# Performance work log

Hardware: AMD Instinct MI355X
Metric: run time of the kernel (lower is better)

## Reference

```python
import jax, jax.numpy as jnp
import numpy as np

B, L_IN, D = 4, 4096, 1024
R_MIN, R_MAX = 0.9, 0.999


def setup_inputs() -> dict:
    key = jax.random.key(0)
    k0, k1, k2 = jax.random.split(key, 3)
    inputs = jax.random.normal(k0, (B, L_IN, D), jnp.float32)
    Wi = jax.random.normal(k1, (2 * D, D), jnp.float32) / np.sqrt(D)
    bi = jnp.zeros((2 * D,), jnp.float32)
    Wo = jax.random.normal(k2, (D, 2 * D), jnp.float32) / np.sqrt(2 * D)
    bo = jnp.zeros((D,), jnp.float32)
    # LRU stable-ring initialization, exactly as in the torch module
    rng = np.random.default_rng(0)
    u1 = rng.random(D)
    u2 = rng.random(D)
    v_log = np.log(-0.5 * np.log(u1 * (R_MAX ** 2 - R_MIN ** 2) + R_MIN ** 2))
    theta_log = np.log(u2 * np.pi * 2)
    gamma_log = np.log(np.sqrt(1.0 - np.exp(-np.exp(v_log)) ** 2))
    params_log = jnp.asarray(np.stack([v_log, theta_log, gamma_log]), jnp.float32)
    return {"inputs": inputs, "Wi": Wi, "bi": bi, "Wo": Wo, "bo": bo,
            "params_log": params_log}


def _lru_forward(inputs, Wi, bi, Wo, bo, params_log):
    b, l_in, d = inputs.shape
    u = inputs @ Wi.T + bi                      # [B, L, 2D]
    v, theta, gamma = jnp.exp(params_log)       # each [D]
    # torch.view_as_complex: interleaved (real, imag) pairs along last dim
    uc = u.reshape(b, l_in, d, 2)
    x = jax.lax.complex(uc[..., 0], uc[..., 1])  # [B, L, D] complex64
    log2_L = int(np.ceil(np.log2(l_in)))
    L = 2 ** log2_L
    x = jnp.pad(x, ((0, 0), (0, L - l_in), (0, 0)))
    # Blelloch-style log-depth scan: x_t = lambda * x_{t-1} + u_t,
    # lambda = exp(-v + i*theta)
    for i in range(1, log2_L + 1):
        blk = 2 ** i
        xb = x.reshape(b * L // blk, blk, d)
        x1, x2 = xb[:, : blk // 2], xb[:, blk // 2:]
        pos = jnp.arange(1, blk // 2 + 1, dtype=jnp.float32)  # [blk/2]
        lambs = jnp.exp(jax.lax.complex(-pos[:, None] * v,
                                        pos[:, None] * theta))  # [blk/2, D]
        x2 = x2 + lambs * x1[:, -1:]
        x = jnp.concatenate([x1, x2], axis=1).reshape(b, L, d)
    x = x[:, :l_in] * gamma.astype(x.dtype)     # normalize, drop padding
    xr = jnp.concatenate([x.real, x.imag], axis=-1)  # [B, L, 2D]
    out = xr @ Wo.T + bo
    return jax.nn.relu(out)


def reference(inputs, Wi, bi, Wo, bo, params_log):
    return _lru_forward(inputs, Wi, bi, Wo, bo, params_log)
```

## Files before the change

### kernel.cpp

```cpp
#include <hip/hip_runtime.h>

#define BB 4
#define LL 4096
#define DD 1024
#define SS2 128
#define TT2 32

typedef __attribute__((ext_vector_type(4))) float  floatx4;
typedef __attribute__((ext_vector_type(8))) short  shortx8;

static __device__ __forceinline__ unsigned short f2bf(float f) {
    unsigned int u = __float_as_uint(f);
    u += 0x7fffu + ((u >> 16) & 1u);
    return (unsigned short)(u >> 16);
}
static __device__ __forceinline__ float bf2f(unsigned short h) {
    return __uint_as_float(((unsigned int)h) << 16);
}

#define NIN4 (BB * LL * DD / 4)
#define NW4  (2 * DD * DD / 4)
__global__ void cast_all_kernel(const float4* __restrict__ s_in, ushort4* __restrict__ d_inb,
                                const float4* __restrict__ s_wi, ushort4* __restrict__ d_wib,
                                const float4* __restrict__ s_wo, ushort4* __restrict__ d_wob) {
    int i = blockIdx.x * blockDim.x + threadIdx.x;
    const float4* s; ushort4* d; int j;
    if (i < NIN4)                 { s = s_in; d = d_inb; j = i; }
    else if (i < NIN4 + NW4)      { s = s_wi; d = d_wib; j = i - NIN4; }
    else                          { s = s_wo; d = d_wob; j = i - NIN4 - NW4; }
    float4 v = s[j];
    ushort4 o;
    o.x = f2bf(v.x); o.y = f2bf(v.y); o.z = f2bf(v.z); o.w = f2bf(v.w);
    d[j] = o;
}

template<int K, int NT, int EPI>
__global__ __launch_bounds__(256)
void gemm_bt(const unsigned short* __restrict__ A,
             const unsigned short* __restrict__ B,
             const float* __restrict__ bias,
             void* __restrict__ Cp) {
    constexpr int N = NT * 128;
    __shared__ __align__(16) short As[128 * 64];
    __shared__ __align__(16) short Bs[128 * 64];

    const int tid = threadIdx.x;
    const int b   = blockIdx.x;
    const int xcd = b & 7;
    const int i2  = b >> 3;
    const int tileM = ((i2 / NT) * 8 + xcd) * 128;
    const int tileN = (i2 % NT) * 128;

    const int lane  = tid & 63;
    const int wave  = tid >> 6;
    const int wm    = (wave >> 1) * 64;
    const int wn    = (wave & 1) * 64;
    const int r16   = lane & 15;
    const int quad  = lane >> 4;

    floatx4 acc[4][4] = {};

    int rowS[4], colS[4];
#pragma unroll
    for (int n = 0; n < 4; ++n) {
        const int q = tid + n * 256;
        rowS[n] = q >> 3;
        colS[n] = ((q & 7) ^ (rowS[n] & 7)) * 8;
    }
    const int ldsBase = (tid & ~63) * 8;

    const int fx = r16 & 7;

    for (int k0 = 0; k0 < K; k0 += 64) {
#pragma unroll
        for (int n = 0; n < 4; ++n) {
            __builtin_amdgcn_global_load_lds(
                (const __attribute__((address_space(1))) void*)&A[(size_t)(tileM + rowS[n]) * K + k0 + colS[n]],
                (__attribute__((address_space(3))) void*)&As[ldsBase + n * 2048], 16, 0, 0);
            __builtin_amdgcn_global_load_lds(
                (const __attribute__((address_space(1))) void*)&B[(size_t)(tileN + rowS[n]) * K + k0 + colS[n]],
                (__attribute__((address_space(3))) void*)&Bs[ldsBase + n * 2048], 16, 0, 0);
        }
        __syncthreads();

#pragma unroll
        for (int kk = 0; kk < 2; ++kk) {
            const int slot = ((kk * 4 + quad) ^ fx) * 8;
            shortx8 af[4], bfv[4];
#pragma unroll
            for (int i = 0; i < 4; ++i)
                af[i] = *(const shortx8*)(&As[(wm + i * 16 + r16) * 64 + slot]);
#pragma unroll
            for (int j = 0; j < 4; ++j)
                bfv[j] = *(const shortx8*)(&Bs[(wn + j * 16 + r16) * 64 + slot]);
#pragma unroll
            for (int i = 0; i < 4; ++i)
#pragma unroll
                for (int j = 0; j < 4; ++j)
                    acc[i][j] = __builtin_amdgcn_mfma_f32_16x16x32_bf16(
                        af[i], bfv[j], acc[i][j], 0, 0, 0);
        }
        __syncthreads();
    }

#pragma unroll
    for (int i = 0; i < 4; ++i) {
#pragma unroll
        for (int j = 0; j < 4; ++j) {
            const int col = tileN + wn + j * 16 + r16;
            const float bv = bias[col];
#pragma unroll
            for (int r = 0; r < 4; ++r) {
                const int row = tileM + wm + i * 16 + quad * 4 + r;
                float v = acc[i][j][r] + bv;
                if (EPI == 0) {
                    ((unsigned short*)Cp)[(size_t)row * N + col] = f2bf(v);
                } else {
                    ((float*)Cp)[(size_t)row * N + col] = fmaxf(v, 0.0f);
                }
            }
        }
    }
}

__global__ __launch_bounds__(256)
void scanA(const unsigned short* __restrict__ u,
           const float* __restrict__ plog,
           float2* __restrict__ Eend) {
    const int d0 = (blockIdx.x * 256 + threadIdx.x) * 2;
    const int c = blockIdx.y, b = blockIdx.z;
    const float v0  = expf(plog[d0]),      v1  = expf(plog[d0 + 1]);
    const float th0 = expf(plog[DD + d0]), th1 = expf(plog[DD + d0 + 1]);
    const float a0 = expf(-v0), a1 = expf(-v1);
    const float lr0 = a0 * cosf(th0), li0 = a0 * sinf(th0);
    const float lr1 = a1 * cosf(th1), li1 = a1 * sinf(th1);

    uint2 uc[TT2];
    const unsigned short* up = u + (size_t)(b * LL + c * TT2) * (2 * DD) + 2 * d0;
#pragma unroll
    for (int t = 0; t < TT2; ++t)
        uc[t] = *(const uint2*)(up + (size_t)t * (2 * DD));

    float zr0 = 0.f, zi0 = 0.f, zr1 = 0.f, zi1 = 0.f;
#pragma unroll
    for (int t = 0; t < TT2; ++t) {
        float xr0 = bf2f((unsigned short)(uc[t].x & 0xffffu));
        float xi0 = bf2f((unsigned short)(uc[t].x >> 16));
        float xr1 = bf2f((unsigned short)(uc[t].y & 0xffffu));
        float xi1 = bf2f((unsigned short)(uc[t].y >> 16));
        float w;
        w = lr0 * zr0 - li0 * zi0 + xr0; zi0 = lr0 * zi0 + li0 * zr0 + xi0; zr0 = w;
        w = lr1 * zr1 - li1 * zi1 + xr1; zi1 = lr1 * zi1 + li1 * zr1 + xi1; zr1 = w;
    }
    *(float4*)&Eend[(size_t)c * (BB * DD) + b * DD + d0] =
        make_float4(zr0, zi0, zr1, zi1);
}

__global__ __launch_bounds__(256)
void scanC(const unsigned short* __restrict__ u,
           const float* __restrict__ plog,
           const float2* __restrict__ Eend,
           unsigned short* __restrict__ xr) {
    const int d0 = (blockIdx.x * 256 + threadIdx.x) * 2;
    const int c = blockIdx.y, b = blockIdx.z;
    const float v0  = expf(plog[d0]),      v1  = expf(plog[d0 + 1]);
    const float th0 = expf(plog[DD + d0]), th1 = expf(plog[DD + d0 + 1]);
    const float g0  = expf(plog[2 * DD + d0]), g1 = expf(plog[2 * DD + d0 + 1]);
    const float a0 = expf(-v0), a1 = expf(-v1);
    const float lr0 = a0 * cosf(th0), li0 = a0 * sinf(th0);
    const float lr1 = a1 * cosf(th1), li1 = a1 * sinf(th1);

    uint2 uc[TT2];
    const unsigned short* up = u + (size_t)(b * LL + c * TT2) * (2 * DD) + 2 * d0;
#pragma unroll
    for (int t = 0; t < TT2; ++t)
        uc[t] = *(const uint2*)(up + (size_t)t * (2 * DD));

    const float aT0 = expf(-(float)TT2 * v0), aT1 = expf(-(float)TT2 * v1);
    const float Lr0 = aT0 * cosf((float)TT2 * th0), Li0 = aT0 * sinf((float)TT2 * th0);
    const float Lr1 = aT1 * cosf((float)TT2 * th1), Li1 = aT1 * sinf((float)TT2 * th1);
    float yr0 = 0.f, yi0 = 0.f, yr1 = 0.f, yi1 = 0.f;
    for (int cc = 0; cc < c; ++cc) {
        float4 e = *(const float4*)&Eend[(size_t)cc * (BB * DD) + b * DD + d0];
        float w;
        w = Lr0 * yr0 - Li0 * yi0 + e.x; yi0 = Lr0 * yi0 + Li0 * yr0 + e.y; yr0 = w;
        w = Lr1 * yr1 - Li1 * yi1 + e.z; yi1 = Lr1 * yi1 + Li1 * yr1 + e.w; yr1 = w;
    }

    unsigned short* xp = xr + (size_t)(b * LL + c * TT2) * (2 * DD) + d0;
#pragma unroll
    for (int t = 0; t < TT2; ++t) {
        float xr0 = bf2f((unsigned short)(uc[t].x & 0xffffu));
        float xi0 = bf2f((unsigned short)(uc[t].x >> 16));
        float xr1 = bf2f((unsigned short)(uc[t].y & 0xffffu));
        float xi1 = bf2f((unsigned short)(uc[t].y >> 16));
        float w;
        w = lr0 * yr0 - li0 * yi0 + xr0; yi0 = lr0 * yi0 + li0 * yr0 + xi0; yr0 = w;
        w = lr1 * yr1 - li1 * yi1 + xr1; yi1 = lr1 * yi1 + li1 * yr1 + xi1; yr1 = w;
        *(unsigned int*)&xp[(size_t)t * (2 * DD)] =
            (unsigned int)f2bf(g0 * yr0) | ((unsigned int)f2bf(g1 * yr1) << 16);
        *(unsigned int*)&xp[(size_t)t * (2 * DD) + DD] =
            (unsigned int)f2bf(g0 * yi0) | ((unsigned int)f2bf(g1 * yi1) << 16);
    }
}

extern "C" void kernel_launch(void* const* d_in, const int* in_sizes, int n_in,
                              void* d_out, int out_size, void* d_ws, size_t ws_size,
                              hipStream_t stream) {
    const float* inputs = (const float*)d_in[0];
    const float* Wi     = (const float*)d_in[1];
    const float* bi     = (const float*)d_in[2];
    const float* Wo     = (const float*)d_in[3];
    const float* bo     = (const float*)d_in[4];
    const float* plog   = (const float*)d_in[5];
    float* out = (float*)d_out;

    const size_t M = (size_t)BB * LL;
    unsigned short* u_bf  = (unsigned short*)d_ws;
    unsigned short* xr_bf = u_bf  + M * 2 * DD;
    unsigned short* in_bf = xr_bf + M * 2 * DD;
    unsigned short* Wi_bf = in_bf + M * DD;
    unsigned short* Wo_bf = Wi_bf + (size_t)2 * DD * DD;
    float2* Eend = (float2*)(Wo_bf + (size_t)2 * DD * DD);

    {
        int total4 = NIN4 + 2 * NW4;
        cast_all_kernel<<<total4 / 256, 256, 0, stream>>>(
            (const float4*)inputs, (ushort4*)in_bf,
            (const float4*)Wi,     (ushort4*)Wi_bf,
            (const float4*)Wo,     (ushort4*)Wo_bf);
    }

    gemm_bt<DD, 16, 0><<<(M / 128) * 16, 256, 0, stream>>>(
        in_bf, Wi_bf, bi, (void*)u_bf);

    scanA<<<dim3(DD / 512, SS2, BB), 256, 0, stream>>>(u_bf, plog, Eend);
    scanC<<<dim3(DD / 512, SS2, BB), 256, 0, stream>>>(u_bf, plog, Eend, xr_bf);

    gemm_bt<2 * DD, 8, 1><<<(M / 128) * 8, 256, 0, stream>>>(
        xr_bf, Wo_bf, bo, (void*)out);
}
```

Measured before the change: 359.7 us.

## Add a chunk-carry scan kernel so scanC reads precomputed carries

Adds a scanB kernel that sequentially scans the per-chunk end states across the 128 chunks once per (batch, channel pair) and writes each chunk's incoming carry. scanC then loads its carry directly instead of re-running a loop over all preceding chunks, which previously gave quadratic total work and uneven load across blocks. The cost is an extra kernel launch, a small serial kernel with only 8 blocks, and extra workspace for the carries.

After: 339.2 us. -5.7%, faster.

```diff
diff --git a/kernel.cpp b/kernel.cpp
--- a/kernel.cpp
+++ b/kernel.cpp
@@ -157,9 +157,43 @@
 }
 
 __global__ __launch_bounds__(256)
+void scanB(const float2* __restrict__ Eend,
+           const float* __restrict__ plog,
+           float2* __restrict__ Cin) {
+    const int idx = blockIdx.x * 256 + threadIdx.x;
+    const int b  = idx / (DD / 2);
+    const int d0 = (idx % (DD / 2)) * 2;
+    const float v0  = expf(plog[d0]),      v1  = expf(plog[d0 + 1]);
+    const float th0 = expf(plog[DD + d0]), th1 = expf(plog[DD + d0 + 1]);
+    const float aT0 = expf(-(float)TT2 * v0), aT1 = expf(-(float)TT2 * v1);
+    const float Lr0 = aT0 * cosf((float)TT2 * th0), Li0 = aT0 * sinf((float)TT2 * th0);
+    const float Lr1 = aT1 * cosf((float)TT2 * th1), Li1 = aT1 * sinf((float)TT2 * th1);
+
+    const size_t base = (size_t)b * DD + d0;
+    float yr0 = 0.f, yi0 = 0.f, yr1 = 0.f, yi1 = 0.f;
+#pragma unroll
+    for (int g = 0; g < SS2 / 16; ++g) {
+        float4 eb[16], cb[16];
+#pragma unroll
+        for (int t = 0; t < 16; ++t)
+            eb[t] = *(const float4*)&Eend[(size_t)(g * 16 + t) * (BB * DD) + base];
+#pragma unroll
+        for (int t = 0; t < 16; ++t) {
+            cb[t] = make_float4(yr0, yi0, yr1, yi1);
+            float w;
+            w = Lr0 * yr0 - Li0 * yi0 + eb[t].x; yi0 = Lr0 * yi0 + Li0 * yr0 + eb[t].y; yr0 = w;
+            w = Lr1 * yr1 - Li1 * yi1 + eb[t].z; yi1 = Lr1 * yi1 + Li1 * yr1 + eb[t].w; yr1 = w;
+        }
+#pragma unroll
+        for (int t = 0; t < 16; ++t)
+            *(float4*)&Cin[(size_t)(g * 16 + t) * (BB * DD) + base] = cb[t];
+    }
+}
+
+__global__ __launch_bounds__(256)
 void scanC(const unsigned short* __restrict__ u,
            const float* __restrict__ plog,
-           const float2* __restrict__ Eend,
+           const float2* __restrict__ Cin,
            unsigned short* __restrict__ xr) {
     const int d0 = (blockIdx.x * 256 + threadIdx.x) * 2;
     const int c = blockIdx.y, b = blockIdx.z;
@@ -176,16 +210,8 @@
     for (int t = 0; t < TT2; ++t)
         uc[t] = *(const uint2*)(up + (size_t)t * (2 * DD));
 
-    const float aT0 = expf(-(float)TT2 * v0), aT1 = expf(-(float)TT2 * v1);
-    const float Lr0 = aT0 * cosf((float)TT2 * th0), Li0 = aT0 * sinf((float)TT2 * th0);
-    const float Lr1 = aT1 * cosf((float)TT2 * th1), Li1 = aT1 * sinf((float)TT2 * th1);
-    float yr0 = 0.f, yi0 = 0.f, yr1 = 0.f, yi1 = 0.f;
-    for (int cc = 0; cc < c; ++cc) {
-        float4 e = *(const float4*)&Eend[(size_t)cc * (BB * DD) + b * DD + d0];
-        float w;
-        w = Lr0 * yr0 - Li0 * yi0 + e.x; yi0 = Lr0 * yi0 + Li0 * yr0 + e.y; yr0 = w;
-        w = Lr1 * yr1 - Li1 * yi1 + e.z; yi1 = Lr1 * yi1 + Li1 * yr1 + e.w; yr1 = w;
-    }
+    float4 cy = *(const float4*)&Cin[(size_t)c * (BB * DD) + b * DD + d0];
+    float yr0 = cy.x, yi0 = cy.y, yr1 = cy.z, yi1 = cy.w;
 
     unsigned short* xp = xr + (size_t)(b * LL + c * TT2) * (2 * DD) + d0;
 #pragma unroll
@@ -222,6 +248,7 @@
     unsigned short* Wi_bf = in_bf + M * DD;
     unsigned short* Wo_bf = Wi_bf + (size_t)2 * DD * DD;
     float2* Eend = (float2*)(Wo_bf + (size_t)2 * DD * DD);
+    float2* Cin  = Eend + (size_t)SS2 * BB * DD;
 
     {
         int total4 = NIN4 + 2 * NW4;
@@ -235,7 +262,8 @@
         in_bf, Wi_bf, bi, (void*)u_bf);
 
     scanA<<<dim3(DD / 512, SS2, BB), 256, 0, stream>>>(u_bf, plog, Eend);
-    scanC<<<dim3(DD / 512, SS2, BB), 256, 0, stream>>>(u_bf, plog, Eend, xr_bf);
+    scanB<<<(BB * DD / 2) / 256, 256, 0, stream>>>(Eend, plog, Cin);
+    scanC<<<dim3(DD / 512, SS2, BB), 256, 0, stream>>>(u_bf, plog, Cin, xr_bf);
 
     gemm_bt<2 * DD, 8, 1><<<(M / 128) * 8, 256, 0, stream>>>(
         xr_bf, Wo_bf, bo, (void*)out);
```
